# Performance work log

Hardware: AMD Instinct MI355X
Metric: run time of the kernel (lower is better)

The kernel has to match this reference:

```python
import jax, jax.numpy as jnp
import numpy as np

TEMPERATURE = 0.07
EPS_NORM = 1e-12   # F.normalize eps
EPS_LOG = 1e-08


def _l2_normalize(x):
    # matches torch.nn.functional.normalize(p=2, dim=1): x / max(||x||, eps)
    n = jnp.sqrt(jnp.sum(x * x, axis=-1, keepdims=True))
    return x / jnp.maximum(n, EPS_NORM)


def setup_inputs() -> dict:
    key = jax.random.key(0)
    k0, k1, k2 = jax.random.split(key, 3)
    B, S, D = 4, 4096, 128
    fea0 = jax.random.normal(k0, (B, S, D), dtype=jnp.float32)
    fea1 = jax.random.normal(k1, (B, S, D), dtype=jnp.float32)
    mask = jax.random.randint(k2, (B, S), 0, 2).astype(jnp.bool_)
    return {"fea0": fea0, "fea1": fea1, "mask": mask}


def reference(fea0, fea1, mask):
    # Equivalent to the torch code: gathering masked rows then building a KxK
    # similarity among them is the same as masking rows/cols of the full NxN
    # matrix (normalization is per-row, independent of the gather).
    D = fea0.shape[-1]
    m = mask.reshape(-1)                       # [N] bool
    f0 = fea0.reshape(-1, D)                   # [N, D]
    f1 = fea1.reshape(-1, D)
    n0 = _l2_normalize(f0)
    n1 = _l2_normalize(f1)
    sim = jnp.einsum('id,jd->ij', n0, n1) / TEMPERATURE   # [N, N]
    exp_sim = jnp.exp(sim)
    numerator = jnp.diagonal(exp_sim)                      # exp(sim_ii)
    denominator = jnp.sum(jnp.where(m[None, :], exp_sim, 0.0), axis=1)
    loss_i = -jnp.log((numerator + EPS_LOG) / (denominator + EPS_LOG))
    cnt = jnp.sum(m.astype(jnp.float32))
    return jnp.sum(jnp.where(m, loss_i, 0.0)) / cnt
```

## Files before the change

### kernel.cpp

```cpp
#include <hip/hip_runtime.h>
#include <hip/hip_bf16.h>


#define DD 128
#define INV_T 14.285714285714286f
#define C_EXP2 20.6099291555566f
#define JSL 4

typedef __attribute__((ext_vector_type(8))) short bf16x8;
typedef __attribute__((ext_vector_type(4))) float f32x4;
typedef unsigned short u16;
typedef unsigned char u8;

__device__ __forceinline__ u16 f2bf(float x) {
    union { float f; unsigned u; } v; v.f = x;
    unsigned r = v.u + 0x7fffu + ((v.u >> 16) & 1u);
    return (u16)(r >> 16);
}

__device__ __forceinline__ float fast_exp2(float x) {
#if __has_builtin(__builtin_amdgcn_exp2f)
    return __builtin_amdgcn_exp2f(x);
#else
    return exp2f(x);
#endif
}

__global__ __launch_bounds__(256) void prep_kernel(
        const u8* __restrict__ mraw, float* __restrict__ maskf,
        float* __restrict__ wc, float* __restrict__ den,
        int* __restrict__ pos, int* __restrict__ cnt, int n) {
    __shared__ int s_any;
    __shared__ int s_wsum[4];
    __shared__ int s_base;
    if (threadIdx.x == 0) s_any = 0;
    __syncthreads();
    int local = 0;
    #pragma unroll
    for (int q = 0; q < 16; ++q) {
        const int p = threadIdx.x * 16 + q;
        if ((p & 3) && mraw[p]) local = 1;
    }
    if (local) atomicOr(&s_any, 1);
    __syncthreads();
    const bool is_u8 = (s_any != 0);
    const int* mi = (const int*)mraw;

    const int i = blockIdx.x * 256 + threadIdx.x;
    const int v = is_u8 ? (int)mraw[i] : mi[i];
    const int m = v ? 1 : 0;
    maskf[i] = (float)m;
    wc[i]   = 0.0f;
    den[i]  = 0.0f;

    const int wave = threadIdx.x >> 6, lane = threadIdx.x & 63;
    const unsigned long long bal = __ballot(m);
    const int wprefix = __popcll(bal & ((1ULL << lane) - 1ULL));
    const int wtotal  = __popcll(bal);
    if (lane == 0) s_wsum[wave] = wtotal;
    __syncthreads();
    if (threadIdx.x == 0)
        s_base = atomicAdd(cnt, s_wsum[0] + s_wsum[1] + s_wsum[2] + s_wsum[3]);
    __syncthreads();
    int wbase = 0;
    #pragma unroll
    for (int w = 0; w < 4; ++w)
        if (w < wave) wbase += s_wsum[w];
    pos[i] = m ? (s_base + wbase + wprefix) : -1;
}

__global__ __launch_bounds__(256) void norm_kernel(
        const float* __restrict__ f0, const float* __restrict__ f1,
        const int* __restrict__ pos,
        u16* __restrict__ n0b, u16* __restrict__ Bc, float* __restrict__ wc,
        float* __restrict__ diag) {
    const int wave = threadIdx.x >> 6, lane = threadIdx.x & 63;
    const int i = blockIdx.x * 4 + wave;
    const float2 a = *(const float2*)(f0 + (size_t)i * DD + lane * 2);
    const float2 b = *(const float2*)(f1 + (size_t)i * DD + lane * 2);
    float s0 = a.x * a.x + a.y * a.y;
    float s1 = b.x * b.x + b.y * b.y;
    float d  = a.x * b.x + a.y * b.y;
    #pragma unroll
    for (int off = 32; off; off >>= 1) {
        s0 += __shfl_xor(s0, off);
        s1 += __shfl_xor(s1, off);
        d  += __shfl_xor(d,  off);
    }
    const float r0 = 1.0f / fmaxf(sqrtf(s0), 1e-12f);
    const float r1 = 1.0f / fmaxf(sqrtf(s1), 1e-12f);
    ushort2 t0; t0.x = f2bf(a.x * r0); t0.y = f2bf(a.y * r0);
    *(ushort2*)(n0b + (size_t)i * DD + lane * 2) = t0;
    const int p = pos[i];
    if (p >= 0) {
        const float sc = r1 * C_EXP2;
        ushort2 t1; t1.x = f2bf(b.x * sc); t1.y = f2bf(b.y * sc);
        *(ushort2*)(Bc + (size_t)p * DD + lane * 2) = t1;
        if (lane == 0) wc[p] = 1.0f;
    }
    if (lane == 0) diag[i] = d * r0 * r1;
}

__device__ __forceinline__ void stage_tile(u16* dst, const u16* src,
                                           int wave, int lane) {
    char* lB = (char*)dst;
    const char* gB = (const char*)src;
    #pragma unroll
    for (int it = 0; it < 8; ++it) {
        const int ldsOff = it * 4096 + wave * 1024;
        const int chunk  = (ldsOff >> 4) + lane;
        const int row    = chunk >> 4;
        const int c      = chunk & 15;
        const int srcOff = row * 256 + ((c ^ (row & 7)) << 4);
        __builtin_amdgcn_global_load_lds(
            (const __attribute__((address_space(1))) unsigned int*)(gB + srcOff),
            (__attribute__((address_space(3))) unsigned int*)(lB + ldsOff),
            16, 0, 0);
    }
}

__global__ __launch_bounds__(256, 2) void gemm_kernel(
        const u16* __restrict__ n0b, const u16* __restrict__ Bc,
        const float* __restrict__ wc, const int* __restrict__ cnt,
        float* __restrict__ den) {
    __shared__ u16 Bs[2][128 * 128];
    const int tid  = threadIdx.x;
    const int wave = tid >> 6, lane = tid & 63;
    const int jsl = blockIdx.x, iblk = blockIdx.y;
    const int wr = wave >> 1, wq = wave & 1;
    const int lr = lane & 15, lk = lane >> 4;

    const int c = *cnt;
    const int ntiles = (c + 127) >> 7;
    const int per = (ntiles + JSL - 1) / JSL;
    const int t0 = jsl * per;
    const int t1 = min(ntiles, t0 + per);

    bf16x8 af[4][4];
    #pragma unroll
    for (int m = 0; m < 4; ++m) {
        const int r = iblk * 128 + wr * 64 + m * 16 + lr;
        const char* rowp = (const char*)(n0b + (size_t)r * DD);
        #pragma unroll
        for (int kk = 0; kk < 4; ++kk)
            af[m][kk] = *(const bf16x8*)(rowp + kk * 64 + lk * 16);
    }

    float dacc[4][4] = {};

    if (t0 < t1) {
        stage_tile(Bs[0], Bc + (size_t)t0 * DD * 128, wave, lane);
        __syncthreads();
        int cur = 0;
        for (int t = t0; t < t1; ++t) {
            if (t + 1 < t1)
                stage_tile(Bs[cur ^ 1], Bc + (size_t)(t + 1) * DD * 128, wave, lane);

            float wv[4];
            #pragma unroll
            for (int nn = 0; nn < 4; ++nn)
                wv[nn] = wc[t * 128 + wq * 64 + nn * 16 + lr];

            f32x4 acc[4][4] = {};
            const char* Bb = (const char*)Bs[cur];
            #pragma unroll
            for (int kk = 0; kk < 4; ++kk) {
                const int byteoff = kk * 64 + lk * 16;
                bf16x8 bfr[4];
                #pragma unroll
                for (int nn = 0; nn < 4; ++nn) {
                    const int rr = wq * 64 + nn * 16 + lr;
                    bfr[nn] = *(const bf16x8*)(Bb + rr * 256 + (byteoff ^ ((rr & 7) << 4)));
                }
                #pragma unroll
                for (int m = 0; m < 4; ++m)
                    #pragma unroll
                    for (int nn = 0; nn < 4; ++nn)
                        acc[m][nn] = __builtin_amdgcn_mfma_f32_16x16x32_bf16(
                                        af[m][kk], bfr[nn], acc[m][nn], 0, 0, 0);
            }

            #pragma unroll
            for (int m = 0; m < 4; ++m)
                #pragma unroll
                for (int reg = 0; reg < 4; ++reg) {
                    float s = dacc[m][reg];
                    #pragma unroll
                    for (int nn = 0; nn < 4; ++nn)
                        s += fast_exp2(acc[m][nn][reg]) * wv[nn];
                    dacc[m][reg] = s;
                }
            __syncthreads();
            cur ^= 1;
        }
    }

    #pragma unroll
    for (int m = 0; m < 4; ++m)
        #pragma unroll
        for (int reg = 0; reg < 4; ++reg) {
            float s = dacc[m][reg];
            s += __shfl_xor(s, 1);
            s += __shfl_xor(s, 2);
            s += __shfl_xor(s, 4);
            s += __shfl_xor(s, 8);
            if (lr == 0)
                atomicAdd(&den[iblk * 128 + wr * 64 + m * 16 + lk * 4 + reg], s);
        }
}

__global__ __launch_bounds__(256) void final1_kernel(
        const float* __restrict__ diag, const float* __restrict__ den,
        const float* __restrict__ maskf, double* __restrict__ accum) {
    const int i = blockIdx.x * 256 + threadIdx.x;
    double ls = 0.0, cs = 0.0;
    const float m = maskf[i];
    if (m != 0.0f) {
        const float num = expf(diag[i] * INV_T);
        const float l = logf(den[i] + 1e-8f) - logf(num + 1e-8f);
        ls = (double)l;
        cs = 1.0;
    }
    #pragma unroll
    for (int off = 32; off; off >>= 1) {
        ls += __shfl_xor(ls, off);
        cs += __shfl_xor(cs, off);
    }
    __shared__ double sl[4], sc[4];
    const int wave = threadIdx.x >> 6, lane = threadIdx.x & 63;
    if (lane == 0) { sl[wave] = ls; sc[wave] = cs; }
    __syncthreads();
    if (threadIdx.x == 0) {
        atomicAdd(&accum[0], sl[0] + sl[1] + sl[2] + sl[3]);
        atomicAdd(&accum[1], sc[0] + sc[1] + sc[2] + sc[3]);
    }
}

__global__ void final2_kernel(const double* __restrict__ accum,
                              float* __restrict__ out) {
    out[0] = (float)(accum[0] / accum[1]);
}

extern "C" void kernel_launch(void* const* d_in, const int* in_sizes, int n_in,
                              void* d_out, int out_size, void* d_ws, size_t ws_size,
                              hipStream_t stream) {
    const float* f0 = (const float*)d_in[0];
    const float* f1 = (const float*)d_in[1];
    const u8*  mraw = (const u8*)d_in[2];
    float* out = (float*)d_out;

    const int N = in_sizes[2];
    char* ws = (char*)d_ws;
    u16*   n0b   = (u16*)ws;
    u16*   Bc    = (u16*)(ws + (size_t)4 * 1024 * 1024);
    float* diag  = (float*)(ws + (size_t)8 * 1024 * 1024);
    float* maskf = diag + N;
    float* wc    = maskf + N;
    float* den   = wc + N;
    int*   pos   = (int*)(den + N);
    int*   cnt   = (int*)(pos + N);
    double* accum = (double*)(cnt + 2);

    hipMemsetAsync(cnt, 0, 2 * sizeof(int) + 2 * sizeof(double), stream);
    prep_kernel<<<N / 256, 256, 0, stream>>>(mraw, maskf, wc, den, pos, cnt, N);
    norm_kernel<<<N / 4, 256, 0, stream>>>(f0, f1, pos, n0b, Bc, wc, diag);
    gemm_kernel<<<dim3(JSL, N / 128), 256, 0, stream>>>(n0b, Bc, wc, cnt, den);
    final1_kernel<<<N / 256, 256, 0, stream>>>(diag, den, maskf, accum);
    final2_kernel<<<1, 1, 0, stream>>>(accum, out);
}
```

Baseline: 118.6 us.

## Drop LDS staging in GEMM, load B fragments per wave, fuse final kernels

The GEMM kernel no longer stages 128x128 B tiles into shared memory with double buffering. Each wave now loads its own 16-column B fragment straight from global memory (relying on L2), shrinks the row block from 128 to 64, and raises launch bounds to allow more blocks per CU. This removes the LDS traffic and barriers but lowers reuse of each B load across rows, so global and L2 traffic grows. Separately, the two final kernels are merged into one, using an atomic ticket so the last block writes the output, which saves one launch.

```diff
diff --git a/kernel.cpp b/kernel.cpp
--- a/kernel.cpp
+++ b/kernel.cpp
@@ -101,98 +101,54 @@
     if (lane == 0) diag[i] = d * r0 * r1;
 }
 
-__device__ __forceinline__ void stage_tile(u16* dst, const u16* src,
-                                           int wave, int lane) {
-    char* lB = (char*)dst;
-    const char* gB = (const char*)src;
-    #pragma unroll
-    for (int it = 0; it < 8; ++it) {
-        const int ldsOff = it * 4096 + wave * 1024;
-        const int chunk  = (ldsOff >> 4) + lane;
-        const int row    = chunk >> 4;
-        const int c      = chunk & 15;
-        const int srcOff = row * 256 + ((c ^ (row & 7)) << 4);
-        __builtin_amdgcn_global_load_lds(
-            (const __attribute__((address_space(1))) unsigned int*)(gB + srcOff),
-            (__attribute__((address_space(3))) unsigned int*)(lB + ldsOff),
-            16, 0, 0);
-    }
-}
-
-__global__ __launch_bounds__(256, 2) void gemm_kernel(
+__global__ __launch_bounds__(256, 4) void gemm_kernel(
         const u16* __restrict__ n0b, const u16* __restrict__ Bc,
         const float* __restrict__ wc, const int* __restrict__ cnt,
         float* __restrict__ den) {
-    __shared__ u16 Bs[2][128 * 128];
     const int tid  = threadIdx.x;
     const int wave = tid >> 6, lane = tid & 63;
-    const int jsl = blockIdx.x, iblk = blockIdx.y;
-    const int wr = wave >> 1, wq = wave & 1;
+    const int bid  = blockIdx.x;
+    const int jsl  = bid & (JSL - 1);
+    const int iblk = bid >> 2;
     const int lr = lane & 15, lk = lane >> 4;
 
     const int c = *cnt;
-    const int ntiles = (c + 127) >> 7;
-    const int per = (ntiles + JSL - 1) / JSL;
-    const int t0 = jsl * per;
-    const int t1 = min(ntiles, t0 + per);
+    const int G = (c + 15) >> 4;
 
     bf16x8 af[4][4];
     #pragma unroll
     for (int m = 0; m < 4; ++m) {
-        const int r = iblk * 128 + wr * 64 + m * 16 + lr;
+        const int r = iblk * 64 + m * 16 + lr;
         const char* rowp = (const char*)(n0b + (size_t)r * DD);
         #pragma unroll
         for (int kk = 0; kk < 4; ++kk)
             af[m][kk] = *(const bf16x8*)(rowp + kk * 64 + lk * 16);
     }
 
-    float dacc[4][4] = {};
-
-    if (t0 < t1) {
-        stage_tile(Bs[0], Bc + (size_t)t0 * DD * 128, wave, lane);
-        __syncthreads();
-        int cur = 0;
-        for (int t = t0; t < t1; ++t) {
-            if (t + 1 < t1)
-                stage_tile(Bs[cur ^ 1], Bc + (size_t)(t + 1) * DD * 128, wave, lane);
-
-            float wv[4];
-            #pragma unroll
-            for (int nn = 0; nn < 4; ++nn)
-                wv[nn] = wc[t * 128 + wq * 64 + nn * 16 + lr];
-
-            f32x4 acc[4][4] = {};
-            const char* Bb = (const char*)Bs[cur];
-            #pragma unroll
-            for (int kk = 0; kk < 4; ++kk) {
-                const int byteoff = kk * 64 + lk * 16;
-                bf16x8 bfr[4];
-                #pragma unroll
-                for (int nn = 0; nn < 4; ++nn) {
-                    const int rr = wq * 64 + nn * 16 + lr;
-                    bfr[nn] = *(const bf16x8*)(Bb + rr * 256 + (byteoff ^ ((rr & 7) << 4)));
-                }
-                #pragma unroll
-                for (int m = 0; m < 4; ++m)
-                    #pragma unroll
-                    for (int nn = 0; nn < 4; ++nn)
-                        acc[m][nn] = __builtin_amdgcn_mfma_f32_16x16x32_bf16(
-                                        af[m][kk], bfr[nn], acc[m][nn], 0, 0, 0);
-            }
-
+    f32x4 dacc[4] = {};
+
+    for (int g = jsl * 4 + wave; g < G; g += 4 * JSL) {
+        const int col = g * 16 + lr;
+        const char* bp = (const char*)(Bc + (size_t)col * DD);
+        bf16x8 bfr[4];
+        #pragma unroll
+        for (int kk = 0; kk < 4; ++kk)
+            bfr[kk] = *(const bf16x8*)(bp + kk * 64 + lk * 16);
+        const float wv = wc[col];
+
+        f32x4 acc[4] = {};
+        #pragma unroll
+        for (int kk = 0; kk < 4; ++kk)
             #pragma unroll
             for (int m = 0; m < 4; ++m)
-                #pragma unroll
-                for (int reg = 0; reg < 4; ++reg) {
-                    float s = dacc[m][reg];
-                    #pragma unroll
-                    for (int nn = 0; nn < 4; ++nn)
-                        s += fast_exp2(acc[m][nn][reg]) * wv[nn];
-                    dacc[m][reg] = s;
-                }
-            __syncthreads();
-            cur ^= 1;
-        }
+                acc[m] = __builtin_amdgcn_mfma_f32_16x16x32_bf16(
+                             af[m][kk], bfr[kk], acc[m], 0, 0, 0);
+
+        #pragma unroll
+        for (int m = 0; m < 4; ++m)
+            #pragma unroll
+            for (int reg = 0; reg < 4; ++reg)
+                dacc[m][reg] += fast_exp2(acc[m][reg]) * wv;
     }
 
     #pragma unroll
@@ -205,13 +161,14 @@
             s += __shfl_xor(s, 4);
             s += __shfl_xor(s, 8);
             if (lr == 0)
-                atomicAdd(&den[iblk * 128 + wr * 64 + m * 16 + lk * 4 + reg], s);
+                atomicAdd(&den[iblk * 64 + m * 16 + lk * 4 + reg], s);
         }
 }
 
-__global__ __launch_bounds__(256) void final1_kernel(
+__global__ __launch_bounds__(256) void final_kernel(
         const float* __restrict__ diag, const float* __restrict__ den,
-        const float* __restrict__ maskf, double* __restrict__ accum) {
+        const float* __restrict__ maskf, double* __restrict__ accum,
+        int* __restrict__ ticket, float* __restrict__ out) {
     const int i = blockIdx.x * 256 + threadIdx.x;
     double ls = 0.0, cs = 0.0;
     const float m = maskf[i];
@@ -233,12 +190,14 @@
     if (threadIdx.x == 0) {
         atomicAdd(&accum[0], sl[0] + sl[1] + sl[2] + sl[3]);
         atomicAdd(&accum[1], sc[0] + sc[1] + sc[2] + sc[3]);
-    }
-}
-
-__global__ void final2_kernel(const double* __restrict__ accum,
-                              float* __restrict__ out) {
-    out[0] = (float)(accum[0] / accum[1]);
+        __threadfence();
+        const int t = atomicAdd(ticket, 1);
+        if (t == (int)gridDim.x - 1) {
+            const double L = atomicAdd(&accum[0], 0.0);
+            const double C = atomicAdd(&accum[1], 0.0);
+            out[0] = (float)(L / C);
+        }
+    }
 }
 
 extern "C" void kernel_launch(void* const* d_in, const int* in_sizes, int n_in,
@@ -259,12 +218,12 @@
     float* den   = wc + N;
     int*   pos   = (int*)(den + N);
     int*   cnt   = (int*)(pos + N);
+    int*   ticket = cnt + 1;
     double* accum = (double*)(cnt + 2);
 
     hipMemsetAsync(cnt, 0, 2 * sizeof(int) + 2 * sizeof(double), stream);
     prep_kernel<<<N / 256, 256, 0, stream>>>(mraw, maskf, wc, den, pos, cnt, N);
     norm_kernel<<<N / 4, 256, 0, stream>>>(f0, f1, pos, n0b, Bc, wc, diag);
-    gemm_kernel<<<dim3(JSL, N / 128), 256, 0, stream>>>(n0b, Bc, wc, cnt, den);
-    final1_kernel<<<N / 256, 256, 0, stream>>>(diag, den, maskf, accum);
-    final2_kernel<<<1, 1, 0, stream>>>(accum, out);
-}
+    gemm_kernel<<<dim3((N / 64) * JSL), 256, 0, stream>>>(n0b, Bc, wc, cnt, den);
+    final_kernel<<<N / 256, 256, 0, stream>>>(diag, den, maskf, accum, ticket, out);
+}
```

Result: slower. 150.9 us (+27.2%).
